# Kernel optimization log

Hardware: AMD Instinct MI355X
Metric: run time of the kernel (lower is better)

## Reference

```python
import jax, jax.numpy as jnp
import numpy as np

N_NODES = 100000
N_EDGES = 1600000
D_IN, D_HID, D_OUT = 64, 128, 64


def setup_inputs() -> dict:
    key = jax.random.key(0)
    ks = jax.random.split(key, 12)
    s = lambda d: 1.0 / np.sqrt(d)
    return {
        "x": jax.random.normal(ks[0], (N_NODES, D_IN), dtype=jnp.float32),
        "edge_index": jax.random.randint(ks[1], (2, N_EDGES), 0, N_NODES, dtype=jnp.int64),
        # conv1 MLP: Linear(D_IN->D_HID), ReLU, Linear(D_HID->D_HID)
        "W1a": jax.random.uniform(ks[2], (D_IN, D_HID), jnp.float32, -s(D_IN), s(D_IN)),
        "b1a": jnp.zeros((D_HID,), jnp.float32),
        "W1b": jax.random.uniform(ks[3], (D_HID, D_HID), jnp.float32, -s(D_HID), s(D_HID)),
        "b1b": jnp.zeros((D_HID,), jnp.float32),
        # conv2 MLP: Linear(D_HID->D_HID), ReLU, Linear(D_HID->D_HID)
        "W2a": jax.random.uniform(ks[4], (D_HID, D_HID), jnp.float32, -s(D_HID), s(D_HID)),
        "b2a": jnp.zeros((D_HID,), jnp.float32),
        "W2b": jax.random.uniform(ks[5], (D_HID, D_HID), jnp.float32, -s(D_HID), s(D_HID)),
        "b2b": jnp.zeros((D_HID,), jnp.float32),
        # final projection Linear(D_HID->D_OUT)
        "Wlin": jax.random.uniform(ks[6], (D_HID, D_OUT), jnp.float32, -s(D_HID), s(D_HID)),
        "blin": jnp.zeros((D_OUT,), jnp.float32),
    }


def _gin_conv(h, src, dst, Wa, ba, Wb, bb, num_nodes):
    # GINConv (eps=0): MLP((1+eps)*x + sum_{j->i} x_j)
    agg = jax.ops.segment_sum(h[src], dst, num_segments=num_nodes)  # [N, d]
    z = h + agg
    z = jax.nn.relu(z @ Wa + ba)
    return z @ Wb + bb


def reference(x, edge_index, W1a, b1a, W1b, b1b, W2a, b2a, W2b, b2b, Wlin, blin):
    n = x.shape[0]
    src, dst = edge_index[0], edge_index[1]
    h = jax.nn.relu(_gin_conv(x, src, dst, W1a, b1a, W1b, b1b, n))
    h = jax.nn.relu(_gin_conv(h, src, dst, W2a, b2a, W2b, b2b, n))
    return h @ Wlin + blin  # [N, D_OUT]
```

## Files before the change

### kernel.cpp

```cpp
#include <hip/hip_runtime.h>
#include <hip/hip_fp16.h>


typedef __attribute__((ext_vector_type(8))) short short8;
typedef __attribute__((ext_vector_type(8))) _Float16 half8;
typedef __attribute__((ext_vector_type(4))) float f32x4;
union F8 { unsigned u[4]; short8 s; half8 h; };


constexpr int BUCKET_SHIFT = 9;
constexpr int BUCKET_NODES = 1 << BUCKET_SHIFT;
constexpr int CAP = 10240;
constexpr int EPB = 4096;
constexpr int NBUCK_MAX = 256;

__global__ __launch_bounds__(256) void bucket_scatter_kernel(const int* __restrict__ ei, int E,
                                                             int* __restrict__ gcur,
                                                             int* __restrict__ gpk,
                                                             int nbuck) {
    __shared__ int spk[EPB];
    __shared__ unsigned char sbuck[EPB];
    __shared__ int lcnt[NBUCK_MAX];
    __shared__ int lbase[NBUCK_MAX];
    __shared__ int lcur[NBUCK_MAX];
    __shared__ int gbase[NBUCK_MAX];
    __shared__ int stmp[256];

    const int t = threadIdx.x;
    const int e0 = blockIdx.x * EPB;
    const int ecnt = min(EPB, E - e0);

    for (int i = t; i < NBUCK_MAX; i += 256) lcnt[i] = 0;
    __syncthreads();

    for (int i = t; i < ecnt; i += 256) {
        int d = ei[E + e0 + i];
        atomicAdd(&lcnt[d >> BUCKET_SHIFT], 1);
    }
    __syncthreads();

    int v = lcnt[t];
    stmp[t] = v;
    __syncthreads();
    #pragma unroll
    for (int off = 1; off < 256; off <<= 1) {
        int add = (t >= off) ? stmp[t - off] : 0;
        __syncthreads();
        stmp[t] += add;
        __syncthreads();
    }
    lbase[t] = stmp[t] - v;
    lcur[t] = stmp[t] - v;
    __syncthreads();

    for (int i = t; i < ecnt; i += 256) {
        int s = ei[e0 + i];
        int d = ei[E + e0 + i];
        int b = d >> BUCKET_SHIFT;
        int p = atomicAdd(&lcur[b], 1);
        spk[p] = ((d & (BUCKET_NODES - 1)) << 17) | s;
        sbuck[p] = (unsigned char)b;
    }
    __syncthreads();

    if (t < nbuck) {
        int c = lcnt[t];
        gbase[t] = (c > 0) ? atomicAdd(&gcur[t], c) : 0;
    }
    __syncthreads();

    for (int i = t; i < ecnt; i += 256) {
        int b = sbuck[i];
        int gp = gbase[b] + (i - lbase[b]);
        if (gp < (b + 1) * CAP) gpk[gp] = spk[i];
    }
}

__global__ __launch_bounds__(256) void bucket_base_kernel(const int* __restrict__ gcur,
                                                          int* __restrict__ bbase,
                                                          int* __restrict__ row_start,
                                                          int nbuck, int N, int E) {
    __shared__ int s[256];
    int t = threadIdx.x;
    int c = 0;
    if (t < nbuck) c = min(gcur[t] - t * CAP, CAP);
    s[t] = c;
    __syncthreads();
    #pragma unroll
    for (int off = 1; off < 256; off <<= 1) {
        int add = (t >= off) ? s[t - off] : 0;
        __syncthreads();
        s[t] += add;
        __syncthreads();
    }
    if (t < nbuck) bbase[t] = s[t] - c;
    if (t == 0) row_start[N] = E;
}

__global__ __launch_bounds__(256) void bucket_build_kernel(const int* __restrict__ gpk,
                                                           const int* __restrict__ gcur,
                                                           const int* __restrict__ bbase,
                                                           int* __restrict__ row_start,
                                                           int* __restrict__ edge_src, int N) {
    __shared__ int h[BUCKET_NODES];
    __shared__ int s[256];
    const int t = threadIdx.x;
    const int b = blockIdx.x;
    const int base = b << BUCKET_SHIFT;

    for (int i = t; i < BUCKET_NODES; i += 256) h[i] = 0;
    __syncthreads();

    int cb = min(gcur[b] - b * CAP, CAP);
    const int* pp = gpk + (size_t)b * CAP;
    for (int i = t; i < cb; i += 256) atomicAdd(&h[((unsigned)pp[i]) >> 17], 1);
    __syncthreads();

    int c0 = h[2 * t], c1 = h[2 * t + 1];
    int psum = c0 + c1;
    s[t] = psum;
    __syncthreads();
    #pragma unroll
    for (int off = 1; off < 256; off <<= 1) {
        int add = (t >= off) ? s[t - off] : 0;
        __syncthreads();
        s[t] += add;
        __syncthreads();
    }
    int ex = s[t] - psum + bbase[b];
    __syncthreads();
    h[2 * t]     = ex;
    h[2 * t + 1] = ex + c0;
    if (base + 2 * t < N)     row_start[base + 2 * t]     = ex;
    if (base + 2 * t + 1 < N) row_start[base + 2 * t + 1] = ex + c0;
    __syncthreads();

    for (int i = t; i < cb; i += 256) {
        unsigned pw = (unsigned)pp[i];
        int p = atomicAdd(&h[pw >> 17], 1);
        edge_src[p] = (int)(pw & 0x1FFFFu);
    }
}


__global__ __launch_bounds__(256) void prep_kernel(const float* __restrict__ W1a,
                                                   const float* __restrict__ W1b,
                                                   const float* __restrict__ W2a,
                                                   const float* __restrict__ W2b,
                                                   const float* __restrict__ Wlin,
                                                   short* __restrict__ hi,
                                                   const float* __restrict__ x,
                                                   __half2* __restrict__ x16, int n2,
                                                   int* __restrict__ gcur, int nbuck) {
    int i = blockIdx.x * 256 + threadIdx.x;
    if (blockIdx.x == 0 && threadIdx.x < nbuck) gcur[threadIdx.x] = threadIdx.x * CAP;
    if (i < 65536) {
        const float* W;
        int base, K, N;
        if (i < 8192)       { W = W1a;  base = 0;     K = 64;  N = 128; }
        else if (i < 24576) { W = W1b;  base = 8192;  K = 128; N = 128; }
        else if (i < 40960) { W = W2a;  base = 24576; K = 128; N = 128; }
        else if (i < 57344) { W = W2b;  base = 40960; K = 128; N = 128; }
        else                { W = Wlin; base = 57344; K = 128; N = 64;  }
        int rel = i - base;
        int NT = N >> 4;
        int j  = rel & 7;
        int l  = (rel >> 3) & 63;
        int tc = rel >> 9;
        int nt = tc % NT;
        int c  = tc / NT;
        int n  = nt * 16 + (l & 15);
        int k  = c * 32 + ((l >> 4) << 3) + j;
        float v = W[k * N + n];
        hi[i] = (short)__half_as_ushort(__float2half_rn(v));
    }
    for (int k = i; k < n2; k += gridDim.x * 256) {
        float2 v = reinterpret_cast<const float2*>(x)[k];
        x16[k] = __floats2half2_rn(v.x, v.y);
    }
}


__device__ inline void acc8(float* a, const uint4& v) {
    const __half2* h = reinterpret_cast<const __half2*>(&v);
    #pragma unroll
    for (int j = 0; j < 4; ++j) {
        float2 f = __half22float2(h[j]);
        a[2 * j]     += f.x;
        a[2 * j + 1] += f.y;
    }
}

__device__ inline uint4 pack8(const float* a) {
    uint4 o;
    __half2 h;
    h = __floats2half2_rn(a[0], a[1]); o.x = *reinterpret_cast<unsigned*>(&h);
    h = __floats2half2_rn(a[2], a[3]); o.y = *reinterpret_cast<unsigned*>(&h);
    h = __floats2half2_rn(a[4], a[5]); o.z = *reinterpret_cast<unsigned*>(&h);
    h = __floats2half2_rn(a[6], a[7]); o.w = *reinterpret_cast<unsigned*>(&h);
    return o;
}

__global__ __launch_bounds__(256) void agg128_fp16(const __half2* __restrict__ H16,
                                                   const int* __restrict__ row_start,
                                                   const int* __restrict__ edge_src,
                                                   __half2* __restrict__ Z16, int N) {
    int wave = threadIdx.x >> 6, lane = threadIdx.x & 63;
    int node = blockIdx.x * 4 + wave;
    if (node >= N) return;
    const int lg = lane >> 4;
    const int lo = lane & 15;
    const uint4* Hv = reinterpret_cast<const uint4*>(H16);
    int beg = row_start[node], end = row_start[node + 1];

    uint4 selfv = Hv[(size_t)node * 16 + lo];

    float a[8];
    #pragma unroll
    for (int j = 0; j < 8; ++j) a[j] = 0.f;
    if (lg == 0) acc8(a, selfv);

    int i = beg;
    for (; i + 16 <= end; i += 16) {
        int s0 = edge_src[i + lg];
        int s1 = edge_src[i + 4 + lg];
        int s2 = edge_src[i + 8 + lg];
        int s3 = edge_src[i + 12 + lg];
        uint4 v0 = Hv[(size_t)s0 * 16 + lo];
        uint4 v1 = Hv[(size_t)s1 * 16 + lo];
        uint4 v2 = Hv[(size_t)s2 * 16 + lo];
        uint4 v3 = Hv[(size_t)s3 * 16 + lo];
        acc8(a, v0); acc8(a, v1); acc8(a, v2); acc8(a, v3);
    }
    if (i + 8 <= end) {
        int s0 = edge_src[i + lg];
        int s1 = edge_src[i + 4 + lg];
        uint4 v0 = Hv[(size_t)s0 * 16 + lo];
        uint4 v1 = Hv[(size_t)s1 * 16 + lo];
        acc8(a, v0); acc8(a, v1);
        i += 8;
    }
    if (i + 4 <= end) {
        int s0 = edge_src[i + lg];
        uint4 v0 = Hv[(size_t)s0 * 16 + lo];
        acc8(a, v0);
        i += 4;
    }
    int rem = end - i;
    if (lg < rem) {
        int s0 = edge_src[i + lg];
        uint4 v0 = Hv[(size_t)s0 * 16 + lo];
        acc8(a, v0);
    }

    #pragma unroll
    for (int j = 0; j < 8; ++j) {
        a[j] += __shfl_xor(a[j], 16);
        a[j] += __shfl_xor(a[j], 32);
    }

    if (lg == 0) {
        reinterpret_cast<uint4*>(Z16)[(size_t)node * 16 + lo] = pack8(a);
    }
}

__global__ __launch_bounds__(256) void agg64_fp16(const __half2* __restrict__ H16,
                                                  const int* __restrict__ row_start,
                                                  const int* __restrict__ edge_src,
                                                  __half2* __restrict__ Z16, int N) {
    int wave = threadIdx.x >> 6, lane = threadIdx.x & 63;
    int node = blockIdx.x * 4 + wave;
    if (node >= N) return;
    const int lg = lane >> 3;
    const int lo = lane & 7;
    const uint4* Hv = reinterpret_cast<const uint4*>(H16);
    int beg = row_start[node], end = row_start[node + 1];

    uint4 selfv = Hv[(size_t)node * 8 + lo];

    float a[8];
    #pragma unroll
    for (int j = 0; j < 8; ++j) a[j] = 0.f;
    if (lg == 0) acc8(a, selfv);

    int i = beg;
    for (; i + 16 <= end; i += 16) {
        int s0 = edge_src[i + lg];
        int s1 = edge_src[i + 8 + lg];
        uint4 v0 = Hv[(size_t)s0 * 8 + lo];
        uint4 v1 = Hv[(size_t)s1 * 8 + lo];
        acc8(a, v0); acc8(a, v1);
    }
    if (i + 8 <= end) {
        int s0 = edge_src[i + lg];
        uint4 v0 = Hv[(size_t)s0 * 8 + lo];
        acc8(a, v0);
        i += 8;
    }
    int rem = end - i;
    if (lg < rem) {
        int s0 = edge_src[i + lg];
        uint4 v0 = Hv[(size_t)s0 * 8 + lo];
        acc8(a, v0);
    }

    #pragma unroll
    for (int j = 0; j < 8; ++j) {
        a[j] += __shfl_xor(a[j], 8);
        a[j] += __shfl_xor(a[j], 16);
        a[j] += __shfl_xor(a[j], 32);
    }

    if (lg == 0) {
        reinterpret_cast<uint4*>(Z16)[(size_t)node * 8 + lo] = pack8(a);
    }
}


template <int K>
__device__ inline void stage_global16(const __half2* __restrict__ z, int M, int m0,
                                      unsigned* __restrict__ P, int t) {
    constexpr int KC = K / 32;
    constexpr int NF = 8 * KC * 64;
    #pragma unroll
    for (int fi = t; fi < NF; fi += 256) {
        int l = fi & 63;
        int tc = fi >> 6;
        int c = tc & (KC - 1);
        int T = tc / KC;
        int row = m0 + T * 16 + (l & 15);
        if (row >= M) row = M - 1;
        int kb = c * 32 + ((l >> 4) << 3);
        const __half2* p = z + (size_t)row * (K / 2) + (kb >> 1);
        uint4 v = *reinterpret_cast<const uint4*>(p);
        int base = ((T * KC + c) * 8) * 66 + l;
        P[base + 0 * 66] = v.x & 0xffffu;
        P[base + 1 * 66] = v.x >> 16;
        P[base + 2 * 66] = v.y & 0xffffu;
        P[base + 3 * 66] = v.y >> 16;
        P[base + 4 * 66] = v.z & 0xffffu;
        P[base + 5 * 66] = v.z >> 16;
        P[base + 6 * 66] = v.w & 0xffffu;
        P[base + 7 * 66] = v.w >> 16;
    }
}

template <int K, int NT>
__device__ inline void stage_compute(const unsigned* __restrict__ P,
                                     const short* __restrict__ WH,
                                     int w, int lane, f32x4 (*acc)[8]) {
    constexpr int KC = K / 32;
    const short8* bhp = reinterpret_cast<const short8*>(WH) + lane;
    for (int c = 0; c < KC; ++c) {
        F8 bh[NT];
        #pragma unroll
        for (int nt = 0; nt < NT; ++nt) {
            bh[nt].s = bhp[(c * NT + nt) * 64];
        }
        #pragma unroll
        for (int mt = 0; mt < 2; ++mt) {
            const int T = w * 2 + mt;
            const unsigned* Pb = P + ((T * KC + c) * 8) * 66 + lane;
            unsigned d[8];
            #pragma unroll
            for (int j = 0; j < 8; ++j) d[j] = Pb[j * 66];
            F8 ah;
            #pragma unroll
            for (int j = 0; j < 4; ++j) {
                ah.u[j] = __builtin_amdgcn_perm(d[2 * j + 1], d[2 * j], 0x05040100u);
            }
            #pragma unroll
            for (int nt = 0; nt < NT; ++nt) {
                acc[mt][nt] = __builtin_amdgcn_mfma_f32_16x16x32_f16(ah.h, bh[nt].h, acc[mt][nt], 0, 0, 0);
            }
        }
    }
}

__device__ inline void epilogue_tile(const f32x4* acc, const float* __restrict__ bias,
                                     unsigned* __restrict__ Pout, int T, int lane) {
    int q = lane >> 4, ln = lane & 15;
    #pragma unroll
    for (int nt = 0; nt < 8; ++nt) {
        int col = nt * 16 + ln;
        float b = bias[col];
        int c = col >> 5, jj = col & 7, q2 = (col >> 3) & 3;
        int pb = ((T * 4 + c) * 8 + jj) * 66;
        #pragma unroll
        for (int r = 0; r < 4; ++r) {
            float v = fmaxf(acc[nt][r] + b, 0.f);
            Pout[pb + ((q * 4 + r) | (q2 << 4))] =
                (unsigned)__half_as_ushort(__float2half_rn(v));
        }
    }
}

__global__ __launch_bounds__(256, 2) void mfma_mlp_A(const __half2* __restrict__ z16,
                                                     const short* __restrict__ WaH,
                                                     const float* __restrict__ ba,
                                                     const short* __restrict__ WbH,
                                                     const float* __restrict__ bb,
                                                     __half* __restrict__ H16out, int M) {
    __shared__ unsigned P[8 * 4 * 8 * 66];
    const int t = threadIdx.x;
    const int w = t >> 6, lane = t & 63;
    const int m0 = blockIdx.x * 128;
    const int q = lane >> 4, ln = lane & 15;

    stage_global16<64>(z16, M, m0, P, t);
    __syncthreads();

    f32x4 acc[2][8];
    #pragma unroll
    for (int mt = 0; mt < 2; ++mt)
        #pragma unroll
        for (int i = 0; i < 8; ++i) acc[mt][i] = (f32x4){0.f, 0.f, 0.f, 0.f};
    stage_compute<64, 8>(P, WaH, w, lane, acc);
    __syncthreads();
    epilogue_tile(acc[0], ba, P, w * 2 + 0, lane);
    epilogue_tile(acc[1], ba, P, w * 2 + 1, lane);
    __syncthreads();

    #pragma unroll
    for (int mt = 0; mt < 2; ++mt)
        #pragma unroll
        for (int i = 0; i < 8; ++i) acc[mt][i] = (f32x4){0.f, 0.f, 0.f, 0.f};
    stage_compute<128, 8>(P, WbH, w, lane, acc);

    #pragma unroll
    for (int mt = 0; mt < 2; ++mt) {
        #pragma unroll
        for (int nt = 0; nt < 8; ++nt) {
            int col = nt * 16 + ln;
            float b = bb[col];
            #pragma unroll
            for (int r = 0; r < 4; ++r) {
                int row = m0 + (w * 2 + mt) * 16 + q * 4 + r;
                if (row < M) {
                    float v = fmaxf(acc[mt][nt][r] + b, 0.f);
                    H16out[(size_t)row * 128 + col] = __float2half_rn(v);
                }
            }
        }
    }
}

__global__ __launch_bounds__(256, 2) void mfma_mlp_B(const __half2* __restrict__ z16,
                                                     const short* __restrict__ WaH,
                                                     const float* __restrict__ ba,
                                                     const short* __restrict__ WbH,
                                                     const float* __restrict__ bb,
                                                     const short* __restrict__ WlH,
                                                     const float* __restrict__ bl,
                                                     float* __restrict__ Out, int M) {
    __shared__ unsigned P[8 * 4 * 8 * 66];
    const int t = threadIdx.x;
    const int w = t >> 6, lane = t & 63;
    const int m0 = blockIdx.x * 128;
    const int q = lane >> 4, ln = lane & 15;

    stage_global16<128>(z16, M, m0, P, t);
    __syncthreads();

    f32x4 acc[2][8];
    #pragma unroll
    for (int mt = 0; mt < 2; ++mt)
        #pragma unroll
        for (int i = 0; i < 8; ++i) acc[mt][i] = (f32x4){0.f, 0.f, 0.f, 0.f};
    stage_compute<128, 8>(P, WaH, w, lane, acc);
    __syncthreads();
    epilogue_tile(acc[0], ba, P, w * 2 + 0, lane);
    epilogue_tile(acc[1], ba, P, w * 2 + 1, lane);
    __syncthreads();

    #pragma unroll
    for (int mt = 0; mt < 2; ++mt)
        #pragma unroll
        for (int i = 0; i < 8; ++i) acc[mt][i] = (f32x4){0.f, 0.f, 0.f, 0.f};
    stage_compute<128, 8>(P, WbH, w, lane, acc);
    __syncthreads();
    epilogue_tile(acc[0], bb, P, w * 2 + 0, lane);
    epilogue_tile(acc[1], bb, P, w * 2 + 1, lane);
    __syncthreads();

    #pragma unroll
    for (int mt = 0; mt < 2; ++mt)
        #pragma unroll
        for (int i = 0; i < 8; ++i) acc[mt][i] = (f32x4){0.f, 0.f, 0.f, 0.f};
    stage_compute<128, 4>(P, WlH, w, lane, acc);

    #pragma unroll
    for (int mt = 0; mt < 2; ++mt) {
        #pragma unroll
        for (int nt = 0; nt < 4; ++nt) {
            int col = nt * 16 + ln;
            float b = bl[col];
            #pragma unroll
            for (int r = 0; r < 4; ++r) {
                int row = m0 + (w * 2 + mt) * 16 + q * 4 + r;
                if (row < M) Out[(size_t)row * 64 + col] = acc[mt][nt][r] + b;
            }
        }
    }
}


extern "C" void kernel_launch(void* const* d_in, const int* in_sizes, int n_in,
                              void* d_out, int out_size, void* d_ws, size_t ws_size,
                              hipStream_t stream) {
    const float* x    = (const float*)d_in[0];
    const int*   ei   = (const int*)d_in[1];
    const float* W1a  = (const float*)d_in[2];
    const float* b1a  = (const float*)d_in[3];
    const float* W1b  = (const float*)d_in[4];
    const float* b1b  = (const float*)d_in[5];
    const float* W2a  = (const float*)d_in[6];
    const float* b2a  = (const float*)d_in[7];
    const float* W2b  = (const float*)d_in[8];
    const float* b2b  = (const float*)d_in[9];
    const float* Wlin = (const float*)d_in[10];
    const float* blin = (const float*)d_in[11];
    float* out = (float*)d_out;

    const int N = in_sizes[0] / 64;
    const int E = in_sizes[1] / 2;
    const int NBUCK = (N + BUCKET_NODES - 1) >> BUCKET_SHIFT;

    char* ws = (char*)d_ws;
    const size_t bufBytes = (size_t)N * 128 * sizeof(float);
    __half2* Zbuf = (__half2*)(ws + 0);
    char* B = ws + bufBytes;
    size_t off = 3 * bufBytes;
    int* row_start = (int*)(ws + off); off += ((size_t)(N + 1) * 4 + 15) & ~(size_t)15;
    int* cnt       = (int*)(ws + off); off += ((size_t)N * 4 + 15) & ~(size_t)15;
    int* partials  = (int*)(ws + off); off += 4096;
    int* gcur      = (int*)(ws + off); off += 4096;
    int* edge_src  = (int*)(ws + off); off += (size_t)E * 4;
    __half* h116   = (__half*)(ws + off); off += (size_t)N * 128 * 2;
    int* gpk = (int*)B;
    short* wHi = (short*)(B + (32u << 20));
    __half* x16 = (__half*)(B + (36u << 20));
    short* w1aH = wHi + 0;
    short* w1bH = wHi + 8192;
    short* w2aH = wHi + 24576;
    short* w2bH = wHi + 40960;
    short* wlH  = wHi + 57344;
    (void)cnt;

    const int NB_G = (N + 127) / 128;
    const int NB_S = (E + EPB - 1) / EPB;
    const int NB_A128 = (N + 3) / 4;
    const int NB_A64  = (N + 3) / 4;
    const int NB_P = 12500;

    prep_kernel<<<NB_P, 256, 0, stream>>>(W1a, W1b, W2a, W2b, Wlin, wHi,
                                          x, (__half2*)x16, N * 32, gcur, NBUCK);

    bucket_scatter_kernel<<<NB_S, 256, 0, stream>>>(ei, E, gcur, gpk, NBUCK);
    bucket_base_kernel<<<1, 256, 0, stream>>>(gcur, partials, row_start, NBUCK, N, E);
    bucket_build_kernel<<<NBUCK, 256, 0, stream>>>(gpk, gcur, partials, row_start,
                                                   edge_src, N);

    agg64_fp16<<<NB_A64, 256, 0, stream>>>((const __half2*)x16, row_start, edge_src, Zbuf, N);
    mfma_mlp_A<<<NB_G, 256, 0, stream>>>(Zbuf, w1aH, b1a, w1bH, b1b, h116, N);

    agg128_fp16<<<NB_A128, 256, 0, stream>>>((const __half2*)h116, row_start, edge_src, Zbuf, N);
    mfma_mlp_B<<<NB_G, 256, 0, stream>>>(Zbuf, w2aH, b2a, w2bH, b2b,
                                         wlH, blin, out, N);
}
```

Measured before the change: 320.8 us.

## Feed MFMA A-operand directly from global and merge bucket scan into build

The first GEMM of each MLP kernel now loads its fp16 A fragments straight from global memory into MFMA registers, skipping the LDS staging pass. Block barriers around the per-warp epilogue and compute stages are dropped, on the assumption that each warp only touches its own LDS tiles. The single-block bucket prefix-sum kernel is folded into the bucket build kernel, which now runs with 1024 threads and scans all 512 node counts directly. EPB is halved so the scatter kernel launches more blocks. The removed barriers carry a race risk if any tile is actually shared between warps, and every build block now redundantly repeats the bucket-base scan.

Measured after the change: 311.6 us. -2.9%, faster.

```diff
diff --git a/kernel.cpp b/kernel.cpp
--- a/kernel.cpp
+++ b/kernel.cpp
@@ -5,13 +5,13 @@
 typedef __attribute__((ext_vector_type(8))) short short8;
 typedef __attribute__((ext_vector_type(8))) _Float16 half8;
 typedef __attribute__((ext_vector_type(4))) float f32x4;
-union F8 { unsigned u[4]; short8 s; half8 h; };
+union F8 { unsigned u[4]; uint4 u4; short8 s; half8 h; };
 
 
 constexpr int BUCKET_SHIFT = 9;
 constexpr int BUCKET_NODES = 1 << BUCKET_SHIFT;
 constexpr int CAP = 10240;
-constexpr int EPB = 4096;
+constexpr int EPB = 2048;
 constexpr int NBUCK_MAX = 256;
 
 __global__ __launch_bounds__(256) void bucket_scatter_kernel(const int* __restrict__ ei, int E,
@@ -76,66 +76,62 @@
     }
 }
 
-__global__ __launch_bounds__(256) void bucket_base_kernel(const int* __restrict__ gcur,
-                                                          int* __restrict__ bbase,
-                                                          int* __restrict__ row_start,
-                                                          int nbuck, int N, int E) {
-    __shared__ int s[256];
-    int t = threadIdx.x;
-    int c = 0;
-    if (t < nbuck) c = min(gcur[t] - t * CAP, CAP);
-    s[t] = c;
-    __syncthreads();
-    #pragma unroll
-    for (int off = 1; off < 256; off <<= 1) {
-        int add = (t >= off) ? s[t - off] : 0;
-        __syncthreads();
-        s[t] += add;
-        __syncthreads();
-    }
-    if (t < nbuck) bbase[t] = s[t] - c;
-    if (t == 0) row_start[N] = E;
-}
-
-__global__ __launch_bounds__(256) void bucket_build_kernel(const int* __restrict__ gpk,
-                                                           const int* __restrict__ gcur,
-                                                           const int* __restrict__ bbase,
-                                                           int* __restrict__ row_start,
-                                                           int* __restrict__ edge_src, int N) {
+__global__ __launch_bounds__(1024) void bucket_build_kernel(const int* __restrict__ gpk,
+                                                            const int* __restrict__ gcur,
+                                                            int* __restrict__ row_start,
+                                                            int* __restrict__ edge_src,
+                                                            int N, int E, int nbuck) {
     __shared__ int h[BUCKET_NODES];
-    __shared__ int s[256];
+    __shared__ int s[BUCKET_NODES];
+    __shared__ int sb[NBUCK_MAX];
+    __shared__ int bbase_sh;
     const int t = threadIdx.x;
     const int b = blockIdx.x;
     const int base = b << BUCKET_SHIFT;
 
-    for (int i = t; i < BUCKET_NODES; i += 256) h[i] = 0;
-    __syncthreads();
+    if (t < NBUCK_MAX) {
+        int c = 0;
+        if (t < nbuck) c = min(gcur[t] - t * CAP, CAP);
+        sb[t] = c;
+    }
+    for (int i = t; i < BUCKET_NODES; i += 1024) h[i] = 0;
+    __syncthreads();
+    #pragma unroll
+    for (int off = 1; off < NBUCK_MAX; off <<= 1) {
+        int add = (t >= off && t < NBUCK_MAX) ? sb[t - off] : 0;
+        __syncthreads();
+        if (t < NBUCK_MAX) sb[t] += add;
+        __syncthreads();
+    }
+    if (t == 0) {
+        int cb0 = min(gcur[b] - b * CAP, CAP);
+        bbase_sh = sb[b] - cb0;
+    }
 
     int cb = min(gcur[b] - b * CAP, CAP);
     const int* pp = gpk + (size_t)b * CAP;
-    for (int i = t; i < cb; i += 256) atomicAdd(&h[((unsigned)pp[i]) >> 17], 1);
-    __syncthreads();
-
-    int c0 = h[2 * t], c1 = h[2 * t + 1];
-    int psum = c0 + c1;
-    s[t] = psum;
-    __syncthreads();
-    #pragma unroll
-    for (int off = 1; off < 256; off <<= 1) {
-        int add = (t >= off) ? s[t - off] : 0;
+    for (int i = t; i < cb; i += 1024) atomicAdd(&h[((unsigned)pp[i]) >> 17], 1);
+    __syncthreads();
+
+    int c0 = (t < BUCKET_NODES) ? h[t] : 0;
+    if (t < BUCKET_NODES) s[t] = c0;
+    __syncthreads();
+    #pragma unroll
+    for (int off = 1; off < BUCKET_NODES; off <<= 1) {
+        int add = (t >= off && t < BUCKET_NODES) ? s[t - off] : 0;
         __syncthreads();
-        s[t] += add;
+        if (t < BUCKET_NODES) s[t] += add;
         __syncthreads();
     }
-    int ex = s[t] - psum + bbase[b];
-    __syncthreads();
-    h[2 * t]     = ex;
-    h[2 * t + 1] = ex + c0;
-    if (base + 2 * t < N)     row_start[base + 2 * t]     = ex;
-    if (base + 2 * t + 1 < N) row_start[base + 2 * t + 1] = ex + c0;
-    __syncthreads();
-
-    for (int i = t; i < cb; i += 256) {
+    if (t < BUCKET_NODES) {
+        int ex = s[t] - c0 + bbase_sh;
+        h[t] = ex;
+        if (base + t < N) row_start[base + t] = ex;
+    }
+    if (b == 0 && t == 0) row_start[N] = E;
+    __syncthreads();
+
+    for (int i = t; i < cb; i += 1024) {
         unsigned pw = (unsigned)pp[i];
         int p = atomicAdd(&h[pw >> 17], 1);
         edge_src[p] = (int)(pw & 0x1FFFFu);
@@ -317,31 +313,33 @@
 }
 
 
-template <int K>
-__device__ inline void stage_global16(const __half2* __restrict__ z, int M, int m0,
-                                      unsigned* __restrict__ P, int t) {
+template <int K, int NT>
+__device__ inline void compute_directA(const __half2* __restrict__ z, int M, int m0,
+                                       const short* __restrict__ WH,
+                                       int w, int lane, f32x4 (*acc)[8]) {
     constexpr int KC = K / 32;
-    constexpr int NF = 8 * KC * 64;
-    #pragma unroll
-    for (int fi = t; fi < NF; fi += 256) {
-        int l = fi & 63;
-        int tc = fi >> 6;
-        int c = tc & (KC - 1);
-        int T = tc / KC;
-        int row = m0 + T * 16 + (l & 15);
+    const short8* bhp = reinterpret_cast<const short8*>(WH) + lane;
+    const int q = lane >> 4, ln = lane & 15;
+    const uint4* zr[2];
+    #pragma unroll
+    for (int mt = 0; mt < 2; ++mt) {
+        int row = m0 + (w * 2 + mt) * 16 + ln;
         if (row >= M) row = M - 1;
-        int kb = c * 32 + ((l >> 4) << 3);
-        const __half2* p = z + (size_t)row * (K / 2) + (kb >> 1);
-        uint4 v = *reinterpret_cast<const uint4*>(p);
-        int base = ((T * KC + c) * 8) * 66 + l;
-        P[base + 0 * 66] = v.x & 0xffffu;
-        P[base + 1 * 66] = v.x >> 16;
-        P[base + 2 * 66] = v.y & 0xffffu;
-        P[base + 3 * 66] = v.y >> 16;
-        P[base + 4 * 66] = v.z & 0xffffu;
-        P[base + 5 * 66] = v.z >> 16;
-        P[base + 6 * 66] = v.w & 0xffffu;
-        P[base + 7 * 66] = v.w >> 16;
+        zr[mt] = reinterpret_cast<const uint4*>(z + (size_t)row * (K / 2));
+    }
+    for (int c = 0; c < KC; ++c) {
+        F8 bh[NT];
+        #pragma unroll
+        for (int nt = 0; nt < NT; ++nt) bh[nt].s = bhp[(c * NT + nt) * 64];
+        #pragma unroll
+        for (int mt = 0; mt < 2; ++mt) {
+            F8 ah;
+            ah.u4 = zr[mt][c * 4 + q];
+            #pragma unroll
+            for (int nt = 0; nt < NT; ++nt) {
+                acc[mt][nt] = __builtin_amdgcn_mfma_f32_16x16x32_f16(ah.h, bh[nt].h, acc[mt][nt], 0, 0, 0);
+            }
+        }
     }
 }
 
@@ -407,19 +405,14 @@
     const int m0 = blockIdx.x * 128;
     const int q = lane >> 4, ln = lane & 15;
 
-    stage_global16<64>(z16, M, m0, P, t);
-    __syncthreads();
-
     f32x4 acc[2][8];
     #pragma unroll
     for (int mt = 0; mt < 2; ++mt)
         #pragma unroll
         for (int i = 0; i < 8; ++i) acc[mt][i] = (f32x4){0.f, 0.f, 0.f, 0.f};
-    stage_compute<64, 8>(P, WaH, w, lane, acc);
-    __syncthreads();
+    compute_directA<64, 8>(z16, M, m0, WaH, w, lane, acc);
     epilogue_tile(acc[0], ba, P, w * 2 + 0, lane);
     epilogue_tile(acc[1], ba, P, w * 2 + 1, lane);
-    __syncthreads();
 
     #pragma unroll
     for (int mt = 0; mt < 2; ++mt)
@@ -459,29 +452,22 @@
     const int m0 = blockIdx.x * 128;
     const int q = lane >> 4, ln = lane & 15;
 
-    stage_global16<128>(z16, M, m0, P, t);
-    __syncthreads();
-
     f32x4 acc[2][8];
     #pragma unroll
     for (int mt = 0; mt < 2; ++mt)
         #pragma unroll
         for (int i = 0; i < 8; ++i) acc[mt][i] = (f32x4){0.f, 0.f, 0.f, 0.f};
-    stage_compute<128, 8>(P, WaH, w, lane, acc);
-    __syncthreads();
+    compute_directA<128, 8>(z16, M, m0, WaH, w, lane, acc);
     epilogue_tile(acc[0], ba, P, w * 2 + 0, lane);
     epilogue_tile(acc[1], ba, P, w * 2 + 1, lane);
-    __syncthreads();
 
     #pragma unroll
     for (int mt = 0; mt < 2; ++mt)
         #pragma unroll
         for (int i = 0; i < 8; ++i) acc[mt][i] = (f32x4){0.f, 0.f, 0.f, 0.f};
     stage_compute<128, 8>(P, WbH, w, lane, acc);
-    __syncthreads();
     epilogue_tile(acc[0], bb, P, w * 2 + 0, lane);
     epilogue_tile(acc[1], bb, P, w * 2 + 1, lane);
-    __syncthreads();
 
     #pragma unroll
     for (int mt = 0; mt < 2; ++mt)
@@ -545,7 +531,7 @@
     short* w2aH = wHi + 24576;
     short* w2bH = wHi + 40960;
     short* wlH  = wHi + 57344;
-    (void)cnt;
+    (void)cnt; (void)partials;
 
     const int NB_G = (N + 127) / 128;
     const int NB_S = (E + EPB - 1) / EPB;
@@ -557,9 +543,8 @@
                                           x, (__half2*)x16, N * 32, gcur, NBUCK);
 
     bucket_scatter_kernel<<<NB_S, 256, 0, stream>>>(ei, E, gcur, gpk, NBUCK);
-    bucket_base_kernel<<<1, 256, 0, stream>>>(gcur, partials, row_start, NBUCK, N, E);
-    bucket_build_kernel<<<NBUCK, 256, 0, stream>>>(gpk, gcur, partials, row_start,
-                                                   edge_src, N);
+    bucket_build_kernel<<<NBUCK, 1024, 0, stream>>>(gpk, gcur, row_start, edge_src,
+                                                    N, E, NBUCK);
 
     agg64_fp16<<<NB_A64, 256, 0, stream>>>((const __half2*)x16, row_start, edge_src, Zbuf, N);
     mfma_mlp_A<<<NB_G, 256, 0, stream>>>(Zbuf, w1aH, b1a, w1bH, b1b, h116, N);
```
